# Kernel tuning notes

Measured on AMD Instinct MI355X. Metric: run time of the kernel, lower is better.

## Reference

```python
import jax, jax.numpy as jnp
import numpy as np

N, NODE_DIM, EDGE_DIM, MSG_DIM, T = 1024, 128, 16, 64, 3
IN_DIM = 2 * NODE_DIM + EDGE_DIM


def setup_inputs() -> dict:
    key = jax.random.key(0)
    ks = jax.random.split(key, 11)
    s = 0.05
    X = jax.random.normal(ks[0], (N, NODE_DIM), jnp.float32)
    A = jax.random.randint(ks[1], (N, N), 0, 2, jnp.int32)  # 0/1 adjacency
    E = jax.random.normal(ks[2], (N, N, EDGE_DIM), jnp.float32)
    # MessageFn MLP params (torch Linear: y = x @ W.T + b)
    W1 = jax.random.normal(ks[3], (MSG_DIM, IN_DIM), jnp.float32) * s
    b1 = jax.random.normal(ks[4], (MSG_DIM,), jnp.float32) * s
    W2 = jax.random.normal(ks[5], (MSG_DIM, MSG_DIM), jnp.float32) * s
    b2 = jax.random.normal(ks[6], (MSG_DIM,), jnp.float32) * s
    # GRUCell params (torch layout: [r|z|n] stacked along rows)
    W_ih = jax.random.normal(ks[7], (3 * NODE_DIM, MSG_DIM), jnp.float32) * s
    b_ih = jax.random.normal(ks[8], (3 * NODE_DIM,), jnp.float32) * s
    W_hh = jax.random.normal(ks[9], (3 * NODE_DIM, NODE_DIM), jnp.float32) * s
    b_hh = jax.random.normal(ks[10], (3 * NODE_DIM,), jnp.float32) * s
    return {"X": X, "A": A, "E": E, "W1": W1, "b1": b1, "W2": W2, "b2": b2,
            "W_ih": W_ih, "b_ih": b_ih, "W_hh": W_hh, "b_hh": b_hh}


def reference(X, A, E, W1, b1, W2, b2, W_ih, b_ih, W_hh, b_hh):
    Amask = A.astype(X.dtype)  # (N, N) 0/1
    # Split first Linear over the concat [h_i, h_j, e_ij]
    Wi = W1[:, :NODE_DIM]
    Wj = W1[:, NODE_DIM:2 * NODE_DIM]
    We = W1[:, 2 * NODE_DIM:]
    # Edge contribution is constant over the T steps: (N, N, msg)
    Ep = jnp.einsum('ije,me->ijm', E, We)
    H = X
    for _ in range(T):
        hi = H @ Wi.T  # (N, msg) -- destination-node contribution
        hj = H @ Wj.T  # (N, msg) -- source-node contribution
        pre = hi[:, None, :] + hj[None, :, :] + Ep + b1  # (N, N, msg)
        msg = jax.nn.relu(pre) @ W2.T + b2               # (N, N, msg)
        # Masked sum over neighbors j (zero vector if no neighbors)
        M = jnp.einsum('ij,ijm->im', Amask, msg)          # (N, msg)
        # GRUCell: h' = (1-z)*n + z*h
        gi = M @ W_ih.T + b_ih
        gh = H @ W_hh.T + b_hh
        gi_r, gi_z, gi_n = jnp.split(gi, 3, axis=-1)
        gh_r, gh_z, gh_n = jnp.split(gh, 3, axis=-1)
        r = jax.nn.sigmoid(gi_r + gh_r)
        z = jax.nn.sigmoid(gi_z + gh_z)
        n = jnp.tanh(gi_n + r * gh_n)
        H = (1.0 - z) * n + z * H
    return H
```

## Files before the change

kernel.cpp:

```cpp
#include <hip/hip_runtime.h>
#include <cstddef>

#define N 1024
#define DN 128
#define DE 16
#define DM 64
#define TSTEPS 3
#define INDIM 272

__global__ __launch_bounds__(256) void kA(const float* __restrict__ H,
                                          const float* __restrict__ W1,
                                          const float* __restrict__ W_hh,
                                          const float* __restrict__ b_hh,
                                          float* __restrict__ P) {
  int i = blockIdx.x;
  int t = threadIdx.x;
  __shared__ float h[DN];
  if (t < DN) h[t] = H[i * DN + t];
  __syncthreads();
  for (int c = t; c < 512; c += 256) {
    const float* w;
    float acc;
    if (c < 64)       { w = W1 + c * INDIM;              acc = 0.f; }
    else if (c < 128) { w = W1 + (c - 64) * INDIM + 128; acc = 0.f; }
    else              { w = W_hh + (c - 128) * DN;       acc = b_hh[c - 128]; }
    const float4* w4 = (const float4*)w;
    #pragma unroll
    for (int k4 = 0; k4 < DN / 4; ++k4) {
      float4 wv = w4[k4];
      acc = fmaf(h[k4 * 4 + 0], wv.x, acc);
      acc = fmaf(h[k4 * 4 + 1], wv.y, acc);
      acc = fmaf(h[k4 * 4 + 2], wv.z, acc);
      acc = fmaf(h[k4 * 4 + 3], wv.w, acc);
    }
    P[i * 512 + c] = acc;
  }
}

__global__ __launch_bounds__(256) void kB(const float* __restrict__ P,
                                          const float* __restrict__ E,
                                          const float* __restrict__ W1,
                                          const float* __restrict__ b1,
                                          const int* __restrict__ A,
                                          float* __restrict__ S,
                                          float* __restrict__ deg) {
  int i  = blockIdx.x;
  int t  = threadIdx.x;
  int mq = t & 15;
  int jj = t >> 4;

  float we[4][16];
  #pragma unroll
  for (int mi = 0; mi < 4; ++mi) {
    const float4* wr4 = (const float4*)(W1 + (size_t)(mq * 4 + mi) * INDIM + 256);
    #pragma unroll
    for (int q = 0; q < 4; ++q) {
      float4 v = wr4[q];
      we[mi][q * 4 + 0] = v.x;
      we[mi][q * 4 + 1] = v.y;
      we[mi][q * 4 + 2] = v.z;
      we[mi][q * 4 + 3] = v.w;
    }
  }

  float hib[4];
  #pragma unroll
  for (int mi = 0; mi < 4; ++mi)
    hib[mi] = P[i * 512 + mq * 4 + mi] + b1[mq * 4 + mi];

  float s[4] = {0.f, 0.f, 0.f, 0.f};
  int degp = 0;

  const float* Erow = E + (size_t)i * N * DE;
  const int*   Arow = A + (size_t)i * N;

  for (int jt = 0; jt < N / 16; ++jt) {
    int j = jt * 16 + jj;

    const float4* e4 = (const float4*)(Erow + (size_t)j * DE);
    float4 q0 = e4[0], q1 = e4[1], q2 = e4[2], q3 = e4[3];
    float ev[16] = {q0.x, q0.y, q0.z, q0.w, q1.x, q1.y, q1.z, q1.w,
                    q2.x, q2.y, q2.z, q2.w, q3.x, q3.y, q3.z, q3.w};

    float4 hj4 = *(const float4*)(P + (size_t)j * 512 + 64 + mq * 4);
    int   a  = Arow[j];
    float af = (float)a;
    if (mq == 0) degp += a;

    float ep[4];
    #pragma unroll
    for (int mi = 0; mi < 4; ++mi) {
      float acc = 0.f;
      #pragma unroll
      for (int e = 0; e < 16; ++e) acc = fmaf(ev[e], we[mi][e], acc);
      ep[mi] = acc;
    }

    float pre0 = hib[0] + hj4.x + ep[0];
    float pre1 = hib[1] + hj4.y + ep[1];
    float pre2 = hib[2] + hj4.z + ep[2];
    float pre3 = hib[3] + hj4.w + ep[3];
    s[0] = fmaf(af, fmaxf(pre0, 0.f), s[0]);
    s[1] = fmaf(af, fmaxf(pre1, 0.f), s[1]);
    s[2] = fmaf(af, fmaxf(pre2, 0.f), s[2]);
    s[3] = fmaf(af, fmaxf(pre3, 0.f), s[3]);
  }

  __shared__ float red[16][DM];
  __shared__ float dred[16];
  *(float4*)&red[jj][mq * 4] = make_float4(s[0], s[1], s[2], s[3]);
  if (mq == 0) dred[jj] = (float)degp;
  __syncthreads();

  if (t < DM) {
    float acc = 0.f;
    #pragma unroll
    for (int r = 0; r < 16; ++r) acc += red[r][t];
    S[(size_t)i * DM + t] = acc;
  }
  if (t == 0) {
    float d = 0.f;
    #pragma unroll
    for (int r = 0; r < 16; ++r) d += dred[r];
    deg[i] = d;
  }
}

__global__ __launch_bounds__(256) void kC(const float* __restrict__ P,
                                          const float* __restrict__ S,
                                          const float* __restrict__ deg,
                                          const float* __restrict__ W2,
                                          const float* __restrict__ b2,
                                          const float* __restrict__ W_ih,
                                          const float* __restrict__ b_ih,
                                          const float* __restrict__ Hin,
                                          float* __restrict__ Hout) {
  int i = blockIdx.x;
  int t = threadIdx.x;
  __shared__ float sS[DM];
  __shared__ float sM[DM];
  __shared__ float sGi[384];

  if (t < DM) sS[t] = S[(size_t)i * DM + t];
  __syncthreads();

  if (t < DM) {
    float acc = deg[i] * b2[t];
    const float4* w4 = (const float4*)(W2 + (size_t)t * DM);
    #pragma unroll
    for (int k4 = 0; k4 < DM / 4; ++k4) {
      float4 wv = w4[k4];
      acc = fmaf(sS[k4 * 4 + 0], wv.x, acc);
      acc = fmaf(sS[k4 * 4 + 1], wv.y, acc);
      acc = fmaf(sS[k4 * 4 + 2], wv.z, acc);
      acc = fmaf(sS[k4 * 4 + 3], wv.w, acc);
    }
    sM[t] = acc;
  }
  __syncthreads();

  for (int c = t; c < 384; c += 256) {
    float acc = b_ih[c];
    const float4* w4 = (const float4*)(W_ih + (size_t)c * DM);
    #pragma unroll
    for (int k4 = 0; k4 < DM / 4; ++k4) {
      float4 wv = w4[k4];
      acc = fmaf(sM[k4 * 4 + 0], wv.x, acc);
      acc = fmaf(sM[k4 * 4 + 1], wv.y, acc);
      acc = fmaf(sM[k4 * 4 + 2], wv.z, acc);
      acc = fmaf(sM[k4 * 4 + 3], wv.w, acc);
    }
    sGi[c] = acc;
  }
  __syncthreads();

  if (t < DN) {
    float ghr = P[(size_t)i * 512 + 128 + t];
    float ghz = P[(size_t)i * 512 + 256 + t];
    float ghn = P[(size_t)i * 512 + 384 + t];
    float gir = sGi[t], giz = sGi[128 + t], gin = sGi[256 + t];
    float r = 1.f / (1.f + expf(-(gir + ghr)));
    float z = 1.f / (1.f + expf(-(giz + ghz)));
    float n = tanhf(gin + r * ghn);
    float h = Hin[(size_t)i * DN + t];
    Hout[(size_t)i * DN + t] = (1.f - z) * n + z * h;
  }
}

extern "C" void kernel_launch(void* const* d_in, const int* in_sizes, int n_in,
                              void* d_out, int out_size, void* d_ws, size_t ws_size,
                              hipStream_t stream) {
  const float* X    = (const float*)d_in[0];
  const int*   A    = (const int*)  d_in[1];
  const float* E    = (const float*)d_in[2];
  const float* W1   = (const float*)d_in[3];
  const float* b1   = (const float*)d_in[4];
  const float* W2   = (const float*)d_in[5];
  const float* b2   = (const float*)d_in[6];
  const float* W_ih = (const float*)d_in[7];
  const float* b_ih = (const float*)d_in[8];
  const float* W_hh = (const float*)d_in[9];
  const float* b_hh = (const float*)d_in[10];
  float* out = (float*)d_out;

  float* ws   = (float*)d_ws;
  float* Hbuf = ws;
  float* P    = Hbuf + N * DN;
  float* S    = P + N * 512;
  float* deg  = S + N * DM;

  hipMemcpyAsync(Hbuf, X, (size_t)N * DN * sizeof(float),
                 hipMemcpyDeviceToDevice, stream);

  for (int step = 0; step < TSTEPS; ++step) {
    kA<<<N, 256, 0, stream>>>(Hbuf, W1, W_hh, b_hh, P);
    kB<<<N, 256, 0, stream>>>(P, E, W1, b1, A, S, deg);
    float* Hout = (step == TSTEPS - 1) ? out : Hbuf;
    kC<<<N, 256, 0, stream>>>(P, S, deg, W2, b2, W_ih, b_ih, Hbuf, Hout);
  }
}
```

Before: 496.9 us.

## Process two nodes per block in projection/GRU kernels and widen edge kernel blocks

Measured after the change: 517.6 us. +4.2%, slower.

```diff
diff --git a/kernel.cpp b/kernel.cpp
--- a/kernel.cpp
+++ b/kernel.cpp
@@ -13,37 +13,43 @@
                                           const float* __restrict__ W_hh,
                                           const float* __restrict__ b_hh,
                                           float* __restrict__ P) {
-  int i = blockIdx.x;
+  int i0 = blockIdx.x * 2;
   int t = threadIdx.x;
-  __shared__ float h[DN];
-  if (t < DN) h[t] = H[i * DN + t];
+  __shared__ float h[2][DN];
+  if (t < 2 * DN) h[t >> 7][t & 127] = H[(size_t)i0 * DN + t];
   __syncthreads();
   for (int c = t; c < 512; c += 256) {
     const float* w;
-    float acc;
-    if (c < 64)       { w = W1 + c * INDIM;              acc = 0.f; }
-    else if (c < 128) { w = W1 + (c - 64) * INDIM + 128; acc = 0.f; }
-    else              { w = W_hh + (c - 128) * DN;       acc = b_hh[c - 128]; }
+    float bias;
+    if (c < 64)       { w = W1 + c * INDIM;              bias = 0.f; }
+    else if (c < 128) { w = W1 + (c - 64) * INDIM + 128; bias = 0.f; }
+    else              { w = W_hh + (c - 128) * DN;       bias = b_hh[c - 128]; }
     const float4* w4 = (const float4*)w;
+    float a0 = bias, a1 = bias;
     #pragma unroll
     for (int k4 = 0; k4 < DN / 4; ++k4) {
       float4 wv = w4[k4];
-      acc = fmaf(h[k4 * 4 + 0], wv.x, acc);
-      acc = fmaf(h[k4 * 4 + 1], wv.y, acc);
-      acc = fmaf(h[k4 * 4 + 2], wv.z, acc);
-      acc = fmaf(h[k4 * 4 + 3], wv.w, acc);
-    }
-    P[i * 512 + c] = acc;
-  }
-}
-
-__global__ __launch_bounds__(256) void kB(const float* __restrict__ P,
-                                          const float* __restrict__ E,
-                                          const float* __restrict__ W1,
-                                          const float* __restrict__ b1,
-                                          const int* __restrict__ A,
-                                          float* __restrict__ S,
-                                          float* __restrict__ deg) {
+      a0 = fmaf(h[0][k4 * 4 + 0], wv.x, a0);
+      a1 = fmaf(h[1][k4 * 4 + 0], wv.x, a1);
+      a0 = fmaf(h[0][k4 * 4 + 1], wv.y, a0);
+      a1 = fmaf(h[1][k4 * 4 + 1], wv.y, a1);
+      a0 = fmaf(h[0][k4 * 4 + 2], wv.z, a0);
+      a1 = fmaf(h[1][k4 * 4 + 2], wv.z, a1);
+      a0 = fmaf(h[0][k4 * 4 + 3], wv.w, a0);
+      a1 = fmaf(h[1][k4 * 4 + 3], wv.w, a1);
+    }
+    P[(size_t)i0 * 512 + c]       = a0;
+    P[(size_t)(i0 + 1) * 512 + c] = a1;
+  }
+}
+
+__global__ __launch_bounds__(1024) void kB(const float* __restrict__ P,
+                                           const float* __restrict__ E,
+                                           const float* __restrict__ W1,
+                                           const float* __restrict__ b1,
+                                           const int* __restrict__ A,
+                                           float* __restrict__ S,
+                                           float* __restrict__ deg) {
   int i  = blockIdx.x;
   int t  = threadIdx.x;
   int mq = t & 15;
@@ -66,7 +72,7 @@
   float hib[4];
   #pragma unroll
   for (int mi = 0; mi < 4; ++mi)
-    hib[mi] = P[i * 512 + mq * 4 + mi] + b1[mq * 4 + mi];
+    hib[mi] = P[(size_t)i * 512 + mq * 4 + mi] + b1[mq * 4 + mi];
 
   float s[4] = {0.f, 0.f, 0.f, 0.f};
   int degp = 0;
@@ -74,13 +80,12 @@
   const float* Erow = E + (size_t)i * N * DE;
   const int*   Arow = A + (size_t)i * N;
 
-  for (int jt = 0; jt < N / 16; ++jt) {
-    int j = jt * 16 + jj;
+  #pragma unroll 2
+  for (int jt = 0; jt < N / 64; ++jt) {
+    int j = jt * 64 + jj;
 
     const float4* e4 = (const float4*)(Erow + (size_t)j * DE);
     float4 q0 = e4[0], q1 = e4[1], q2 = e4[2], q3 = e4[3];
-    float ev[16] = {q0.x, q0.y, q0.z, q0.w, q1.x, q1.y, q1.z, q1.w,
-                    q2.x, q2.y, q2.z, q2.w, q3.x, q3.y, q3.z, q3.w};
 
     float4 hj4 = *(const float4*)(P + (size_t)j * 512 + 64 + mq * 4);
     int   a  = Arow[j];
@@ -90,9 +95,23 @@
     float ep[4];
     #pragma unroll
     for (int mi = 0; mi < 4; ++mi) {
-      float acc = 0.f;
-      #pragma unroll
-      for (int e = 0; e < 16; ++e) acc = fmaf(ev[e], we[mi][e], acc);
+      float acc;
+      acc = q0.x * we[mi][0];
+      acc = fmaf(q0.y, we[mi][1], acc);
+      acc = fmaf(q0.z, we[mi][2], acc);
+      acc = fmaf(q0.w, we[mi][3], acc);
+      acc = fmaf(q1.x, we[mi][4], acc);
+      acc = fmaf(q1.y, we[mi][5], acc);
+      acc = fmaf(q1.z, we[mi][6], acc);
+      acc = fmaf(q1.w, we[mi][7], acc);
+      acc = fmaf(q2.x, we[mi][8], acc);
+      acc = fmaf(q2.y, we[mi][9], acc);
+      acc = fmaf(q2.z, we[mi][10], acc);
+      acc = fmaf(q2.w, we[mi][11], acc);
+      acc = fmaf(q3.x, we[mi][12], acc);
+      acc = fmaf(q3.y, we[mi][13], acc);
+      acc = fmaf(q3.z, we[mi][14], acc);
+      acc = fmaf(q3.w, we[mi][15], acc);
       ep[mi] = acc;
     }
 
@@ -106,8 +125,8 @@
     s[3] = fmaf(af, fmaxf(pre3, 0.f), s[3]);
   }
 
-  __shared__ float red[16][DM];
-  __shared__ float dred[16];
+  __shared__ float red[64][DM];
+  __shared__ float dred[64];
   *(float4*)&red[jj][mq * 4] = make_float4(s[0], s[1], s[2], s[3]);
   if (mq == 0) dred[jj] = (float)degp;
   __syncthreads();
@@ -115,13 +134,13 @@
   if (t < DM) {
     float acc = 0.f;
     #pragma unroll
-    for (int r = 0; r < 16; ++r) acc += red[r][t];
+    for (int r = 0; r < 64; ++r) acc += red[r][t];
     S[(size_t)i * DM + t] = acc;
   }
-  if (t == 0) {
+  if (t == DM) {
     float d = 0.f;
     #pragma unroll
-    for (int r = 0; r < 16; ++r) d += dred[r];
+    for (int r = 0; r < 64; ++r) d += dred[r];
     deg[i] = d;
   }
 }
@@ -135,55 +154,64 @@
                                           const float* __restrict__ b_ih,
                                           const float* __restrict__ Hin,
                                           float* __restrict__ Hout) {
-  int i = blockIdx.x;
+  int i0 = blockIdx.x * 2;
   int t = threadIdx.x;
-  __shared__ float sS[DM];
-  __shared__ float sM[DM];
-  __shared__ float sGi[384];
-
-  if (t < DM) sS[t] = S[(size_t)i * DM + t];
-  __syncthreads();
-
-  if (t < DM) {
-    float acc = deg[i] * b2[t];
-    const float4* w4 = (const float4*)(W2 + (size_t)t * DM);
+  __shared__ float sS[2][DM];
+  __shared__ float sM[2][DM];
+  __shared__ float sGi[2][384];
+
+  if (t < 2 * DM) sS[t >> 6][t & 63] = S[(size_t)i0 * DM + t];
+  __syncthreads();
+
+  if (t < 2 * DM) {
+    int ii = t >> 6, m = t & 63;
+    float acc = deg[i0 + ii] * b2[m];
+    const float4* w4 = (const float4*)(W2 + (size_t)m * DM);
     #pragma unroll
     for (int k4 = 0; k4 < DM / 4; ++k4) {
       float4 wv = w4[k4];
-      acc = fmaf(sS[k4 * 4 + 0], wv.x, acc);
-      acc = fmaf(sS[k4 * 4 + 1], wv.y, acc);
-      acc = fmaf(sS[k4 * 4 + 2], wv.z, acc);
-      acc = fmaf(sS[k4 * 4 + 3], wv.w, acc);
-    }
-    sM[t] = acc;
+      acc = fmaf(sS[ii][k4 * 4 + 0], wv.x, acc);
+      acc = fmaf(sS[ii][k4 * 4 + 1], wv.y, acc);
+      acc = fmaf(sS[ii][k4 * 4 + 2], wv.z, acc);
+      acc = fmaf(sS[ii][k4 * 4 + 3], wv.w, acc);
+    }
+    sM[ii][m] = acc;
   }
   __syncthreads();
 
   for (int c = t; c < 384; c += 256) {
-    float acc = b_ih[c];
+    float b = b_ih[c];
+    float a0 = b, a1 = b;
     const float4* w4 = (const float4*)(W_ih + (size_t)c * DM);
     #pragma unroll
     for (int k4 = 0; k4 < DM / 4; ++k4) {
       float4 wv = w4[k4];
-      acc = fmaf(sM[k4 * 4 + 0], wv.x, acc);
-      acc = fmaf(sM[k4 * 4 + 1], wv.y, acc);
-      acc = fmaf(sM[k4 * 4 + 2], wv.z, acc);
-      acc = fmaf(sM[k4 * 4 + 3], wv.w, acc);
-    }
-    sGi[c] = acc;
-  }
-  __syncthreads();
-
-  if (t < DN) {
-    float ghr = P[(size_t)i * 512 + 128 + t];
-    float ghz = P[(size_t)i * 512 + 256 + t];
-    float ghn = P[(size_t)i * 512 + 384 + t];
-    float gir = sGi[t], giz = sGi[128 + t], gin = sGi[256 + t];
+      a0 = fmaf(sM[0][k4 * 4 + 0], wv.x, a0);
+      a1 = fmaf(sM[1][k4 * 4 + 0], wv.x, a1);
+      a0 = fmaf(sM[0][k4 * 4 + 1], wv.y, a0);
+      a1 = fmaf(sM[1][k4 * 4 + 1], wv.y, a1);
+      a0 = fmaf(sM[0][k4 * 4 + 2], wv.z, a0);
+      a1 = fmaf(sM[1][k4 * 4 + 2], wv.z, a1);
+      a0 = fmaf(sM[0][k4 * 4 + 3], wv.w, a0);
+      a1 = fmaf(sM[1][k4 * 4 + 3], wv.w, a1);
+    }
+    sGi[0][c] = a0;
+    sGi[1][c] = a1;
+  }
+  __syncthreads();
+
+  {
+    int ii = t >> 7, tt = t & 127;
+    int i = i0 + ii;
+    float ghr = P[(size_t)i * 512 + 128 + tt];
+    float ghz = P[(size_t)i * 512 + 256 + tt];
+    float ghn = P[(size_t)i * 512 + 384 + tt];
+    float gir = sGi[ii][tt], giz = sGi[ii][128 + tt], gin = sGi[ii][256 + tt];
     float r = 1.f / (1.f + expf(-(gir + ghr)));
     float z = 1.f / (1.f + expf(-(giz + ghz)));
     float n = tanhf(gin + r * ghn);
-    float h = Hin[(size_t)i * DN + t];
-    Hout[(size_t)i * DN + t] = (1.f - z) * n + z * h;
+    float h = Hin[(size_t)i * DN + tt];
+    Hout[(size_t)i * DN + tt] = (1.f - z) * n + z * h;
   }
 }
 
@@ -213,9 +241,9 @@
                  hipMemcpyDeviceToDevice, stream);
 
   for (int step = 0; step < TSTEPS; ++step) {
-    kA<<<N, 256, 0, stream>>>(Hbuf, W1, W_hh, b_hh, P);
-    kB<<<N, 256, 0, stream>>>(P, E, W1, b1, A, S, deg);
+    kA<<<N / 2, 256, 0, stream>>>(Hbuf, W1, W_hh, b_hh, P);
+    kB<<<N, 1024, 0, stream>>>(P, E, W1, b1, A, S, deg);
     float* Hout = (step == TSTEPS - 1) ? out : Hbuf;
-    kC<<<N, 256, 0, stream>>>(P, S, deg, W2, b2, W_ih, b_ih, Hbuf, Hout);
-  }
-}
+    kC<<<N / 2, 256, 0, stream>>>(P, S, deg, W2, b2, W_ih, b_ih, Hbuf, Hout);
+  }
+}
```

## Fuse per-step kernels into one with next-step projections and double-buffered P

Applied to the files above, without the earlier changes.

Result: slower. 611.6 us (+23.1%).

```diff
diff --git a/kernel.cpp b/kernel.cpp
--- a/kernel.cpp
+++ b/kernel.cpp
@@ -8,144 +8,146 @@
 #define TSTEPS 3
 #define INDIM 272
 
-__global__ __launch_bounds__(256) void kA(const float* __restrict__ H,
-                                          const float* __restrict__ W1,
-                                          const float* __restrict__ W_hh,
-                                          const float* __restrict__ b_hh,
-                                          float* __restrict__ P) {
+__global__ __launch_bounds__(512, 4) void kInit(const float* __restrict__ H,
+                                                const float* __restrict__ W1,
+                                                const float* __restrict__ W_hh,
+                                                const float* __restrict__ b_hh,
+                                                float* __restrict__ P) {
   int i = blockIdx.x;
   int t = threadIdx.x;
   __shared__ float h[DN];
-  if (t < DN) h[t] = H[i * DN + t];
-  __syncthreads();
-  for (int c = t; c < 512; c += 256) {
-    const float* w;
-    float acc;
-    if (c < 64)       { w = W1 + c * INDIM;              acc = 0.f; }
-    else if (c < 128) { w = W1 + (c - 64) * INDIM + 128; acc = 0.f; }
-    else              { w = W_hh + (c - 128) * DN;       acc = b_hh[c - 128]; }
-    const float4* w4 = (const float4*)w;
-    #pragma unroll
-    for (int k4 = 0; k4 < DN / 4; ++k4) {
-      float4 wv = w4[k4];
-      acc = fmaf(h[k4 * 4 + 0], wv.x, acc);
-      acc = fmaf(h[k4 * 4 + 1], wv.y, acc);
-      acc = fmaf(h[k4 * 4 + 2], wv.z, acc);
-      acc = fmaf(h[k4 * 4 + 3], wv.w, acc);
-    }
-    P[i * 512 + c] = acc;
-  }
+  if (t < DN) h[t] = H[(size_t)i * DN + t];
+  __syncthreads();
+
+  const float* w;
+  float acc;
+  if (t < 64)       { w = W1 + (size_t)t * INDIM;              acc = 0.f; }
+  else if (t < 128) { w = W1 + (size_t)(t - 64) * INDIM + 128; acc = 0.f; }
+  else              { w = W_hh + (size_t)(t - 128) * DN;       acc = b_hh[t - 128]; }
+  const float4* w4 = (const float4*)w;
+  float a0 = 0.f, a1 = 0.f;
+  #pragma unroll
+  for (int k4 = 0; k4 < DN / 8; ++k4) {
+    float4 wv0 = w4[2 * k4];
+    float4 wv1 = w4[2 * k4 + 1];
+    a0 = fmaf(h[k4 * 8 + 0], wv0.x, a0);
+    a1 = fmaf(h[k4 * 8 + 4], wv1.x, a1);
+    a0 = fmaf(h[k4 * 8 + 1], wv0.y, a0);
+    a1 = fmaf(h[k4 * 8 + 5], wv1.y, a1);
+    a0 = fmaf(h[k4 * 8 + 2], wv0.z, a0);
+    a1 = fmaf(h[k4 * 8 + 6], wv1.z, a1);
+    a0 = fmaf(h[k4 * 8 + 3], wv0.w, a0);
+    a1 = fmaf(h[k4 * 8 + 7], wv1.w, a1);
+  }
+  P[(size_t)i * 512 + t] = acc + a0 + a1;
 }
 
-__global__ __launch_bounds__(256) void kB(const float* __restrict__ P,
-                                          const float* __restrict__ E,
-                                          const float* __restrict__ W1,
-                                          const float* __restrict__ b1,
-                                          const int* __restrict__ A,
-                                          float* __restrict__ S,
-                                          float* __restrict__ deg) {
+__global__ __launch_bounds__(512, 4) void kStep(const float* __restrict__ Pcur,
+                                                const float* __restrict__ E,
+                                                const float* __restrict__ W1,
+                                                const float* __restrict__ b1,
+                                                const int* __restrict__ A,
+                                                const float* __restrict__ W2,
+                                                const float* __restrict__ b2,
+                                                const float* __restrict__ W_ih,
+                                                const float* __restrict__ b_ih,
+                                                const float* __restrict__ W_hh,
+                                                const float* __restrict__ b_hh,
+                                                const float* __restrict__ Hin,
+                                                float* __restrict__ Hout,
+                                                float* __restrict__ Pnext,
+                                                int doPA) {
   int i  = blockIdx.x;
   int t  = threadIdx.x;
-  int mq = t & 15;
-  int jj = t >> 4;
-
-  float we[4][16];
-  #pragma unroll
-  for (int mi = 0; mi < 4; ++mi) {
-    const float4* wr4 = (const float4*)(W1 + (size_t)(mq * 4 + mi) * INDIM + 256);
-    #pragma unroll
-    for (int q = 0; q < 4; ++q) {
-      float4 v = wr4[q];
-      we[mi][q * 4 + 0] = v.x;
-      we[mi][q * 4 + 1] = v.y;
-      we[mi][q * 4 + 2] = v.z;
-      we[mi][q * 4 + 3] = v.w;
-    }
-  }
-
-  float hib[4];
-  #pragma unroll
-  for (int mi = 0; mi < 4; ++mi)
-    hib[mi] = P[i * 512 + mq * 4 + mi] + b1[mq * 4 + mi];
-
-  float s[4] = {0.f, 0.f, 0.f, 0.f};
-  int degp = 0;
-
-  const float* Erow = E + (size_t)i * N * DE;
-  const int*   Arow = A + (size_t)i * N;
-
-  for (int jt = 0; jt < N / 16; ++jt) {
-    int j = jt * 16 + jj;
-
-    const float4* e4 = (const float4*)(Erow + (size_t)j * DE);
-    float4 q0 = e4[0], q1 = e4[1], q2 = e4[2], q3 = e4[3];
-    float ev[16] = {q0.x, q0.y, q0.z, q0.w, q1.x, q1.y, q1.z, q1.w,
-                    q2.x, q2.y, q2.z, q2.w, q3.x, q3.y, q3.z, q3.w};
-
-    float4 hj4 = *(const float4*)(P + (size_t)j * 512 + 64 + mq * 4);
-    int   a  = Arow[j];
-    float af = (float)a;
-    if (mq == 0) degp += a;
-
-    float ep[4];
-    #pragma unroll
-    for (int mi = 0; mi < 4; ++mi) {
-      float acc = 0.f;
-      #pragma unroll
-      for (int e = 0; e < 16; ++e) acc = fmaf(ev[e], we[mi][e], acc);
-      ep[mi] = acc;
-    }
-
-    float pre0 = hib[0] + hj4.x + ep[0];
-    float pre1 = hib[1] + hj4.y + ep[1];
-    float pre2 = hib[2] + hj4.z + ep[2];
-    float pre3 = hib[3] + hj4.w + ep[3];
-    s[0] = fmaf(af, fmaxf(pre0, 0.f), s[0]);
-    s[1] = fmaf(af, fmaxf(pre1, 0.f), s[1]);
-    s[2] = fmaf(af, fmaxf(pre2, 0.f), s[2]);
-    s[3] = fmaf(af, fmaxf(pre3, 0.f), s[3]);
-  }
-
-  __shared__ float red[16][DM];
-  __shared__ float dred[16];
-  *(float4*)&red[jj][mq * 4] = make_float4(s[0], s[1], s[2], s[3]);
-  if (mq == 0) dred[jj] = (float)degp;
-  __syncthreads();
-
-  if (t < DM) {
-    float acc = 0.f;
-    #pragma unroll
-    for (int r = 0; r < 16; ++r) acc += red[r][t];
-    S[(size_t)i * DM + t] = acc;
-  }
-  if (t == 0) {
-    float d = 0.f;
-    #pragma unroll
-    for (int r = 0; r < 16; ++r) d += dred[r];
-    deg[i] = d;
-  }
-}
-
-__global__ __launch_bounds__(256) void kC(const float* __restrict__ P,
-                                          const float* __restrict__ S,
-                                          const float* __restrict__ deg,
-                                          const float* __restrict__ W2,
-                                          const float* __restrict__ b2,
-                                          const float* __restrict__ W_ih,
-                                          const float* __restrict__ b_ih,
-                                          const float* __restrict__ Hin,
-                                          float* __restrict__ Hout) {
-  int i = blockIdx.x;
-  int t = threadIdx.x;
+  int m  = t & 63;
+  int jg = t >> 6;
+
+  __shared__ int   sA[N];
+  __shared__ float red[8][DM];
+  __shared__ float dred[8];
   __shared__ float sS[DM];
   __shared__ float sM[DM];
   __shared__ float sGi[384];
-
-  if (t < DM) sS[t] = S[(size_t)i * DM + t];
+  __shared__ float sH[DN];
+  __shared__ float sdeg;
+
+  const int* Arow = A + (size_t)i * N;
+  sA[t]       = Arow[t];
+  sA[t + 512] = Arow[t + 512];
+
+  float we[16];
+  {
+    const float4* wr4 = (const float4*)(W1 + (size_t)m * INDIM + 256);
+    #pragma unroll
+    for (int q = 0; q < 4; ++q) {
+      float4 v = wr4[q];
+      we[q * 4 + 0] = v.x;
+      we[q * 4 + 1] = v.y;
+      we[q * 4 + 2] = v.z;
+      we[q * 4 + 3] = v.w;
+    }
+  }
+  float hib = Pcur[(size_t)i * 512 + m] + b1[m];
+
+  __syncthreads();
+
+  float s = 0.f;
+  int   dg = 0;
+
+  const float4* e4  = (const float4*)(E + ((size_t)i * N + jg) * DE);
+  const float*  hjp = Pcur + (size_t)jg * 512 + 64 + m;
+
+  #pragma unroll 2
+  for (int jt = 0; jt < N / 8; ++jt) {
+    float4 q0 = e4[0], q1 = e4[1], q2 = e4[2], q3 = e4[3];
+    float  hj = *hjp;
+    int    a  = sA[jt * 8 + jg];
+    if (m == 0) dg += a;
+
+    float acc = hib + hj;
+    acc = fmaf(q0.x, we[0],  acc);
+    acc = fmaf(q0.y, we[1],  acc);
+    acc = fmaf(q0.z, we[2],  acc);
+    acc = fmaf(q0.w, we[3],  acc);
+    acc = fmaf(q1.x, we[4],  acc);
+    acc = fmaf(q1.y, we[5],  acc);
+    acc = fmaf(q1.z, we[6],  acc);
+    acc = fmaf(q1.w, we[7],  acc);
+    acc = fmaf(q2.x, we[8],  acc);
+    acc = fmaf(q2.y, we[9],  acc);
+    acc = fmaf(q2.z, we[10], acc);
+    acc = fmaf(q2.w, we[11], acc);
+    acc = fmaf(q3.x, we[12], acc);
+    acc = fmaf(q3.y, we[13], acc);
+    acc = fmaf(q3.z, we[14], acc);
+    acc = fmaf(q3.w, we[15], acc);
+
+    s = fmaf((float)a, fmaxf(acc, 0.f), s);
+
+    e4  += 8 * DE / 4;
+    hjp += 8 * 512;
+  }
+
+  red[jg][m] = s;
+  if (m == 0) dred[jg] = (float)dg;
   __syncthreads();
 
   if (t < DM) {
-    float acc = deg[i] * b2[t];
+    float acc = 0.f;
+    #pragma unroll
+    for (int r = 0; r < 8; ++r) acc += red[r][t];
+    sS[t] = acc;
+  }
+  if (t == DM) {
+    float d = 0.f;
+    #pragma unroll
+    for (int r = 0; r < 8; ++r) d += dred[r];
+    sdeg = d;
+  }
+  __syncthreads();
+
+  if (t < DM) {
+    float acc = sdeg * b2[t];
     const float4* w4 = (const float4*)(W2 + (size_t)t * DM);
     #pragma unroll
     for (int k4 = 0; k4 < DM / 4; ++k4) {
@@ -159,9 +161,9 @@
   }
   __syncthreads();
 
-  for (int c = t; c < 384; c += 256) {
-    float acc = b_ih[c];
-    const float4* w4 = (const float4*)(W_ih + (size_t)c * DM);
+  if (t < 384) {
+    float acc = b_ih[t];
+    const float4* w4 = (const float4*)(W_ih + (size_t)t * DM);
     #pragma unroll
     for (int k4 = 0; k4 < DM / 4; ++k4) {
       float4 wv = w4[k4];
@@ -170,20 +172,47 @@
       acc = fmaf(sM[k4 * 4 + 2], wv.z, acc);
       acc = fmaf(sM[k4 * 4 + 3], wv.w, acc);
     }
-    sGi[c] = acc;
+    sGi[t] = acc;
   }
   __syncthreads();
 
   if (t < DN) {
-    float ghr = P[(size_t)i * 512 + 128 + t];
-    float ghz = P[(size_t)i * 512 + 256 + t];
-    float ghn = P[(size_t)i * 512 + 384 + t];
+    float ghr = Pcur[(size_t)i * 512 + 128 + t];
+    float ghz = Pcur[(size_t)i * 512 + 256 + t];
+    float ghn = Pcur[(size_t)i * 512 + 384 + t];
     float gir = sGi[t], giz = sGi[128 + t], gin = sGi[256 + t];
     float r = 1.f / (1.f + expf(-(gir + ghr)));
     float z = 1.f / (1.f + expf(-(giz + ghz)));
     float n = tanhf(gin + r * ghn);
     float h = Hin[(size_t)i * DN + t];
-    Hout[(size_t)i * DN + t] = (1.f - z) * n + z * h;
+    float hn = (1.f - z) * n + z * h;
+    sH[t] = hn;
+    Hout[(size_t)i * DN + t] = hn;
+  }
+  __syncthreads();
+
+  if (doPA) {
+    const float* w;
+    float acc;
+    if (t < 64)       { w = W1 + (size_t)t * INDIM;              acc = 0.f; }
+    else if (t < 128) { w = W1 + (size_t)(t - 64) * INDIM + 128; acc = 0.f; }
+    else              { w = W_hh + (size_t)(t - 128) * DN;       acc = b_hh[t - 128]; }
+    const float4* w4 = (const float4*)w;
+    float a0 = 0.f, a1 = 0.f;
+    #pragma unroll
+    for (int k4 = 0; k4 < DN / 8; ++k4) {
+      float4 wv0 = w4[2 * k4];
+      float4 wv1 = w4[2 * k4 + 1];
+      a0 = fmaf(sH[k4 * 8 + 0], wv0.x, a0);
+      a1 = fmaf(sH[k4 * 8 + 4], wv1.x, a1);
+      a0 = fmaf(sH[k4 * 8 + 1], wv0.y, a0);
+      a1 = fmaf(sH[k4 * 8 + 5], wv1.y, a1);
+      a0 = fmaf(sH[k4 * 8 + 2], wv0.z, a0);
+      a1 = fmaf(sH[k4 * 8 + 6], wv1.z, a1);
+      a0 = fmaf(sH[k4 * 8 + 3], wv0.w, a0);
+      a1 = fmaf(sH[k4 * 8 + 7], wv1.w, a1);
+    }
+    Pnext[(size_t)i * 512 + t] = acc + a0 + a1;
   }
 }
 
@@ -205,17 +234,20 @@
 
   float* ws   = (float*)d_ws;
   float* Hbuf = ws;
-  float* P    = Hbuf + N * DN;
-  float* S    = P + N * 512;
-  float* deg  = S + N * DM;
-
-  hipMemcpyAsync(Hbuf, X, (size_t)N * DN * sizeof(float),
-                 hipMemcpyDeviceToDevice, stream);
-
+  float* P0   = Hbuf + N * DN;
+  float* P1   = P0 + N * 512;
+
+  kInit<<<N, 512, 0, stream>>>(X, W1, W_hh, b_hh, P0);
+
+  const float* Hin = X;
+  float* Pc = P0;
+  float* Pn = P1;
   for (int step = 0; step < TSTEPS; ++step) {
-    kA<<<N, 256, 0, stream>>>(Hbuf, W1, W_hh, b_hh, P);
-    kB<<<N, 256, 0, stream>>>(P, E, W1, b1, A, S, deg);
-    float* Hout = (step == TSTEPS - 1) ? out : Hbuf;
-    kC<<<N, 256, 0, stream>>>(P, S, deg, W2, b2, W_ih, b_ih, Hbuf, Hout);
+    int last = (step == TSTEPS - 1);
+    float* Hout = last ? out : Hbuf;
+    kStep<<<N, 512, 0, stream>>>(Pc, E, W1, b1, A, W2, b2, W_ih, b_ih,
+                                 W_hh, b_hh, Hin, Hout, Pn, last ? 0 : 1);
+    Hin = Hbuf;
+    float* tmp = Pc; Pc = Pn; Pn = tmp;
   }
 }
```

## Split edge kernel across neighbor chunks with partial sums and restructure thread mapping

Applied to the files above, without the earlier changes.

Result: slower. 561.3 us (+13.0%).

```diff
diff --git a/kernel.cpp b/kernel.cpp
--- a/kernel.cpp
+++ b/kernel.cpp
@@ -8,144 +8,196 @@
 #define TSTEPS 3
 #define INDIM 272
 
-__global__ __launch_bounds__(256) void kA(const float* __restrict__ H,
-                                          const float* __restrict__ W1,
-                                          const float* __restrict__ W_hh,
-                                          const float* __restrict__ b_hh,
-                                          float* __restrict__ P) {
-  int i = blockIdx.x;
+__global__ __launch_bounds__(256, 8) void kA(const float* __restrict__ H,
+                                             const float* __restrict__ W1,
+                                             const float* __restrict__ W_hh,
+                                             const float* __restrict__ b_hh,
+                                             float* __restrict__ P) {
+  int b = blockIdx.x;
+  int i = b >> 1;
   int t = threadIdx.x;
+  int c = ((b & 1) << 8) + t;
+
   __shared__ float h[DN];
-  if (t < DN) h[t] = H[i * DN + t];
-  __syncthreads();
-  for (int c = t; c < 512; c += 256) {
-    const float* w;
-    float acc;
-    if (c < 64)       { w = W1 + c * INDIM;              acc = 0.f; }
-    else if (c < 128) { w = W1 + (c - 64) * INDIM + 128; acc = 0.f; }
-    else              { w = W_hh + (c - 128) * DN;       acc = b_hh[c - 128]; }
-    const float4* w4 = (const float4*)w;
-    #pragma unroll
-    for (int k4 = 0; k4 < DN / 4; ++k4) {
-      float4 wv = w4[k4];
-      acc = fmaf(h[k4 * 4 + 0], wv.x, acc);
-      acc = fmaf(h[k4 * 4 + 1], wv.y, acc);
-      acc = fmaf(h[k4 * 4 + 2], wv.z, acc);
-      acc = fmaf(h[k4 * 4 + 3], wv.w, acc);
-    }
-    P[i * 512 + c] = acc;
-  }
-}
-
-__global__ __launch_bounds__(256) void kB(const float* __restrict__ P,
-                                          const float* __restrict__ E,
-                                          const float* __restrict__ W1,
-                                          const float* __restrict__ b1,
-                                          const int* __restrict__ A,
-                                          float* __restrict__ S,
-                                          float* __restrict__ deg) {
-  int i  = blockIdx.x;
+  if (t < DN) h[t] = H[(size_t)i * DN + t];
+  __syncthreads();
+
+  const float* w;
+  float bias = 0.f;
+  if (c < 64)       { w = W1 + (size_t)c * INDIM; }
+  else if (c < 128) { w = W1 + (size_t)(c - 64) * INDIM + 128; }
+  else              { w = W_hh + (size_t)(c - 128) * DN; bias = b_hh[c - 128]; }
+  const float4* w4 = (const float4*)w;
+
+  float a0 = bias, a1 = 0.f;
+  #pragma unroll
+  for (int k = 0; k < 16; ++k) {
+    float4 wv0 = w4[2 * k];
+    float4 wv1 = w4[2 * k + 1];
+    a0 = fmaf(h[8 * k + 0], wv0.x, a0);
+    a1 = fmaf(h[8 * k + 4], wv1.x, a1);
+    a0 = fmaf(h[8 * k + 1], wv0.y, a0);
+    a1 = fmaf(h[8 * k + 5], wv1.y, a1);
+    a0 = fmaf(h[8 * k + 2], wv0.z, a0);
+    a1 = fmaf(h[8 * k + 6], wv1.z, a1);
+    a0 = fmaf(h[8 * k + 3], wv0.w, a0);
+    a1 = fmaf(h[8 * k + 7], wv1.w, a1);
+  }
+  P[(size_t)i * 512 + c] = a0 + a1;
+}
+
+__global__ __launch_bounds__(256, 5) void kB(const float* __restrict__ P,
+                                             const float* __restrict__ E,
+                                             const float* __restrict__ W1,
+                                             const float* __restrict__ b1,
+                                             const int* __restrict__ A,
+                                             float* __restrict__ S_part,
+                                             float* __restrict__ deg_part) {
+  int b  = blockIdx.x;
+  int i  = b >> 2;
+  int p  = b & 3;
+  int jbase = p << 8;
   int t  = threadIdx.x;
-  int mq = t & 15;
-  int jj = t >> 4;
-
-  float we[4][16];
-  #pragma unroll
-  for (int mi = 0; mi < 4; ++mi) {
-    const float4* wr4 = (const float4*)(W1 + (size_t)(mq * 4 + mi) * INDIM + 256);
+  int mh = t & 31;
+  int jj = t >> 5;
+  int m0 = mh << 1;
+
+  __shared__ float sAf[256];
+  __shared__ float red[8][DM];
+
+  sAf[t] = (float)A[(size_t)i * N + jbase + t];
+
+  float we0[16], we1[16];
+  {
+    const float4* wr0 = (const float4*)(W1 + (size_t)m0 * INDIM + 256);
+    const float4* wr1 = (const float4*)(W1 + (size_t)(m0 + 1) * INDIM + 256);
     #pragma unroll
     for (int q = 0; q < 4; ++q) {
-      float4 v = wr4[q];
-      we[mi][q * 4 + 0] = v.x;
-      we[mi][q * 4 + 1] = v.y;
-      we[mi][q * 4 + 2] = v.z;
-      we[mi][q * 4 + 3] = v.w;
-    }
-  }
-
-  float hib[4];
-  #pragma unroll
-  for (int mi = 0; mi < 4; ++mi)
-    hib[mi] = P[i * 512 + mq * 4 + mi] + b1[mq * 4 + mi];
-
-  float s[4] = {0.f, 0.f, 0.f, 0.f};
-  int degp = 0;
-
-  const float* Erow = E + (size_t)i * N * DE;
-  const int*   Arow = A + (size_t)i * N;
-
-  for (int jt = 0; jt < N / 16; ++jt) {
-    int j = jt * 16 + jj;
-
-    const float4* e4 = (const float4*)(Erow + (size_t)j * DE);
-    float4 q0 = e4[0], q1 = e4[1], q2 = e4[2], q3 = e4[3];
-    float ev[16] = {q0.x, q0.y, q0.z, q0.w, q1.x, q1.y, q1.z, q1.w,
-                    q2.x, q2.y, q2.z, q2.w, q3.x, q3.y, q3.z, q3.w};
-
-    float4 hj4 = *(const float4*)(P + (size_t)j * 512 + 64 + mq * 4);
-    int   a  = Arow[j];
-    float af = (float)a;
-    if (mq == 0) degp += a;
-
-    float ep[4];
-    #pragma unroll
-    for (int mi = 0; mi < 4; ++mi) {
-      float acc = 0.f;
-      #pragma unroll
-      for (int e = 0; e < 16; ++e) acc = fmaf(ev[e], we[mi][e], acc);
-      ep[mi] = acc;
-    }
-
-    float pre0 = hib[0] + hj4.x + ep[0];
-    float pre1 = hib[1] + hj4.y + ep[1];
-    float pre2 = hib[2] + hj4.z + ep[2];
-    float pre3 = hib[3] + hj4.w + ep[3];
-    s[0] = fmaf(af, fmaxf(pre0, 0.f), s[0]);
-    s[1] = fmaf(af, fmaxf(pre1, 0.f), s[1]);
-    s[2] = fmaf(af, fmaxf(pre2, 0.f), s[2]);
-    s[3] = fmaf(af, fmaxf(pre3, 0.f), s[3]);
-  }
-
-  __shared__ float red[16][DM];
-  __shared__ float dred[16];
-  *(float4*)&red[jj][mq * 4] = make_float4(s[0], s[1], s[2], s[3]);
-  if (mq == 0) dred[jj] = (float)degp;
+      float4 v0 = wr0[q];
+      float4 v1 = wr1[q];
+      we0[4 * q + 0] = v0.x; we1[4 * q + 0] = v1.x;
+      we0[4 * q + 1] = v0.y; we1[4 * q + 1] = v1.y;
+      we0[4 * q + 2] = v0.z; we1[4 * q + 2] = v1.z;
+      we0[4 * q + 3] = v0.w; we1[4 * q + 3] = v1.w;
+    }
+  }
+  float hib0 = P[(size_t)i * 512 + m0]     + b1[m0];
+  float hib1 = P[(size_t)i * 512 + m0 + 1] + b1[m0 + 1];
+
+  __syncthreads();
+
+  float s0 = 0.f, s1 = 0.f;
+  const float* Eb = E + ((size_t)i * N + jbase) * DE;
+
+  for (int g = 0; g < 16; ++g) {
+    float4 e0q0, e0q1, e0q2, e0q3, e1q0, e1q1, e1q2, e1q3;
+    float2 hj0, hj1;
+    float  a0, a1;
+    int jl0 = (g << 4) + jj;
+    int jl1 = jl0 + 8;
+    {
+      const float4* e4 = (const float4*)(Eb + (size_t)jl0 * DE);
+      e0q0 = e4[0]; e0q1 = e4[1]; e0q2 = e4[2]; e0q3 = e4[3];
+    }
+    {
+      const float4* e4 = (const float4*)(Eb + (size_t)jl1 * DE);
+      e1q0 = e4[0]; e1q1 = e4[1]; e1q2 = e4[2]; e1q3 = e4[3];
+    }
+    hj0 = *(const float2*)(P + (size_t)(jbase + jl0) * 512 + 64 + m0);
+    hj1 = *(const float2*)(P + (size_t)(jbase + jl1) * 512 + 64 + m0);
+    a0 = sAf[jl0];
+    a1 = sAf[jl1];
+
+    {
+      float c0 = hib0 + hj0.x;
+      float c1 = hib1 + hj0.y;
+      c0 = fmaf(e0q0.x, we0[0],  c0); c1 = fmaf(e0q0.x, we1[0],  c1);
+      c0 = fmaf(e0q0.y, we0[1],  c0); c1 = fmaf(e0q0.y, we1[1],  c1);
+      c0 = fmaf(e0q0.z, we0[2],  c0); c1 = fmaf(e0q0.z, we1[2],  c1);
+      c0 = fmaf(e0q0.w, we0[3],  c0); c1 = fmaf(e0q0.w, we1[3],  c1);
+      c0 = fmaf(e0q1.x, we0[4],  c0); c1 = fmaf(e0q1.x, we1[4],  c1);
+      c0 = fmaf(e0q1.y, we0[5],  c0); c1 = fmaf(e0q1.y, we1[5],  c1);
+      c0 = fmaf(e0q1.z, we0[6],  c0); c1 = fmaf(e0q1.z, we1[6],  c1);
+      c0 = fmaf(e0q1.w, we0[7],  c0); c1 = fmaf(e0q1.w, we1[7],  c1);
+      c0 = fmaf(e0q2.x, we0[8],  c0); c1 = fmaf(e0q2.x, we1[8],  c1);
+      c0 = fmaf(e0q2.y, we0[9],  c0); c1 = fmaf(e0q2.y, we1[9],  c1);
+      c0 = fmaf(e0q2.z, we0[10], c0); c1 = fmaf(e0q2.z, we1[10], c1);
+      c0 = fmaf(e0q2.w, we0[11], c0); c1 = fmaf(e0q2.w, we1[11], c1);
+      c0 = fmaf(e0q3.x, we0[12], c0); c1 = fmaf(e0q3.x, we1[12], c1);
+      c0 = fmaf(e0q3.y, we0[13], c0); c1 = fmaf(e0q3.y, we1[13], c1);
+      c0 = fmaf(e0q3.z, we0[14], c0); c1 = fmaf(e0q3.z, we1[14], c1);
+      c0 = fmaf(e0q3.w, we0[15], c0); c1 = fmaf(e0q3.w, we1[15], c1);
+      s0 = fmaf(a0, fmaxf(c0, 0.f), s0);
+      s1 = fmaf(a0, fmaxf(c1, 0.f), s1);
+    }
+    {
+      float c0 = hib0 + hj1.x;
+      float c1 = hib1 + hj1.y;
+      c0 = fmaf(e1q0.x, we0[0],  c0); c1 = fmaf(e1q0.x, we1[0],  c1);
+      c0 = fmaf(e1q0.y, we0[1],  c0); c1 = fmaf(e1q0.y, we1[1],  c1);
+      c0 = fmaf(e1q0.z, we0[2],  c0); c1 = fmaf(e1q0.z, we1[2],  c1);
+      c0 = fmaf(e1q0.w, we0[3],  c0); c1 = fmaf(e1q0.w, we1[3],  c1);
+      c0 = fmaf(e1q1.x, we0[4],  c0); c1 = fmaf(e1q1.x, we1[4],  c1);
+      c0 = fmaf(e1q1.y, we0[5],  c0); c1 = fmaf(e1q1.y, we1[5],  c1);
+      c0 = fmaf(e1q1.z, we0[6],  c0); c1 = fmaf(e1q1.z, we1[6],  c1);
+      c0 = fmaf(e1q1.w, we0[7],  c0); c1 = fmaf(e1q1.w, we1[7],  c1);
+      c0 = fmaf(e1q2.x, we0[8],  c0); c1 = fmaf(e1q2.x, we1[8],  c1);
+      c0 = fmaf(e1q2.y, we0[9],  c0); c1 = fmaf(e1q2.y, we1[9],  c1);
+      c0 = fmaf(e1q2.z, we0[10], c0); c1 = fmaf(e1q2.z, we1[10], c1);
+      c0 = fmaf(e1q2.w, we0[11], c0); c1 = fmaf(e1q2.w, we1[11], c1);
+      c0 = fmaf(e1q3.x, we0[12], c0); c1 = fmaf(e1q3.x, we1[12], c1);
+      c0 = fmaf(e1q3.y, we0[13], c0); c1 = fmaf(e1q3.y, we1[13], c1);
+      c0 = fmaf(e1q3.z, we0[14], c0); c1 = fmaf(e1q3.z, we1[14], c1);
+      c0 = fmaf(e1q3.w, we0[15], c0); c1 = fmaf(e1q3.w, we1[15], c1);
+      s0 = fmaf(a1, fmaxf(c0, 0.f), s0);
+      s1 = fmaf(a1, fmaxf(c1, 0.f), s1);
+    }
+  }
+
+  *(float2*)&red[jj][m0] = make_float2(s0, s1);
   __syncthreads();
 
   if (t < DM) {
-    float acc = 0.f;
-    #pragma unroll
-    for (int r = 0; r < 16; ++r) acc += red[r][t];
-    S[(size_t)i * DM + t] = acc;
-  }
-  if (t == 0) {
-    float d = 0.f;
-    #pragma unroll
-    for (int r = 0; r < 16; ++r) d += dred[r];
-    deg[i] = d;
-  }
-}
-
-__global__ __launch_bounds__(256) void kC(const float* __restrict__ P,
-                                          const float* __restrict__ S,
-                                          const float* __restrict__ deg,
-                                          const float* __restrict__ W2,
-                                          const float* __restrict__ b2,
-                                          const float* __restrict__ W_ih,
-                                          const float* __restrict__ b_ih,
-                                          const float* __restrict__ Hin,
-                                          float* __restrict__ Hout) {
+    float acc = red[0][t] + red[1][t] + red[2][t] + red[3][t]
+              + red[4][t] + red[5][t] + red[6][t] + red[7][t];
+    S_part[((size_t)(i << 2) + p) * DM + t] = acc;
+  }
+  if (t < 64) {
+    float d = sAf[t] + sAf[t + 64] + sAf[t + 128] + sAf[t + 192];
+    #pragma unroll
+    for (int off = 32; off > 0; off >>= 1) d += __shfl_down(d, off);
+    if (t == 0) deg_part[(i << 2) + p] = d;
+  }
+}
+
+__global__ __launch_bounds__(256, 4) void kC(const float* __restrict__ P,
+                                             const float* __restrict__ S_part,
+                                             const float* __restrict__ deg_part,
+                                             const float* __restrict__ W2,
+                                             const float* __restrict__ b2,
+                                             const float* __restrict__ W_ih,
+                                             const float* __restrict__ b_ih,
+                                             const float* __restrict__ Hin,
+                                             float* __restrict__ Hout) {
   int i = blockIdx.x;
   int t = threadIdx.x;
   __shared__ float sS[DM];
   __shared__ float sM[DM];
   __shared__ float sGi[384];
-
-  if (t < DM) sS[t] = S[(size_t)i * DM + t];
-  __syncthreads();
+  __shared__ float sdeg;
 
   if (t < DM) {
-    float acc = deg[i] * b2[t];
+    const float* sp = S_part + ((size_t)i << 2) * DM + t;
+    sS[t] = sp[0] + sp[DM] + sp[2 * DM] + sp[3 * DM];
+  }
+  if (t == 64) {
+    const float* dp = deg_part + ((size_t)i << 2);
+    sdeg = dp[0] + dp[1] + dp[2] + dp[3];
+  }
+  __syncthreads();
+
+  if (t < DM) {
+    float acc = sdeg * b2[t];
     const float4* w4 = (const float4*)(W2 + (size_t)t * DM);
     #pragma unroll
     for (int k4 = 0; k4 < DM / 4; ++k4) {
@@ -203,19 +255,20 @@
   const float* b_hh = (const float*)d_in[10];
   float* out = (float*)d_out;
 
-  float* ws   = (float*)d_ws;
-  float* Hbuf = ws;
-  float* P    = Hbuf + N * DN;
-  float* S    = P + N * 512;
-  float* deg  = S + N * DM;
-
-  hipMemcpyAsync(Hbuf, X, (size_t)N * DN * sizeof(float),
-                 hipMemcpyDeviceToDevice, stream);
-
+  float* ws       = (float*)d_ws;
+  float* P        = ws;
+  float* S_part   = P + (size_t)N * 512;
+  float* deg_part = S_part + (size_t)N * 4 * DM;
+  float* Hbuf     = deg_part + 4096;
+
+  const float* Hcur = X;
   for (int step = 0; step < TSTEPS; ++step) {
-    kA<<<N, 256, 0, stream>>>(Hbuf, W1, W_hh, b_hh, P);
-    kB<<<N, 256, 0, stream>>>(P, E, W1, b1, A, S, deg);
-    float* Hout = (step == TSTEPS - 1) ? out : Hbuf;
-    kC<<<N, 256, 0, stream>>>(P, S, deg, W2, b2, W_ih, b_ih, Hbuf, Hout);
-  }
-}
+    int last = (step == TSTEPS - 1);
+    kA<<<2048, 256, 0, stream>>>(Hcur, W1, W_hh, b_hh, P);
+    kB<<<4096, 256, 0, stream>>>(P, E, W1, b1, A, S_part, deg_part);
+    float* Hout = last ? out : Hbuf;
+    kC<<<1024, 256, 0, stream>>>(P, S_part, deg_part, W2, b2, W_ih, b_ih,
+                                 Hcur, Hout);
+    Hcur = Hout;
+  }
+}
```
